# Kernel tuning notes

Hardware: AMD Instinct MI355X
Metric: run time of the kernel (lower is better)

The kernel has to match this reference:

```python
import jax, jax.numpy as jnp
import numpy as np

H = 96  # LSTM units hardcoded in the module


def setup_inputs() -> dict:
    key = jax.random.key(0)
    ks = jax.random.split(key, 5)
    B, LAT, V = 32, 64, 10000
    z = jax.random.normal(ks[0], (B, LAT), dtype=jnp.float32)
    # Keras LSTM params: kernel [in,4H], recurrent_kernel [H,4H], bias [4H]; gate order i,f,c,o
    W = jax.random.normal(ks[1], (LAT, 4 * H), dtype=jnp.float32) * 0.05
    U = jax.random.normal(ks[2], (H, 4 * H), dtype=jnp.float32) * 0.05
    b = jnp.zeros((4 * H,), dtype=jnp.float32)
    Wd = jax.random.normal(ks[3], (H, V), dtype=jnp.float32) * 0.05
    bd = jnp.zeros((V,), dtype=jnp.float32)
    return {"z": z, "W": W, "U": U, "b": b, "Wd": Wd, "bd": bd, "seq_len": 512}


def reference(z, W, U, b, Wd, bd, seq_len):
    # RepeatVector: every timestep sees the same input z, so the input
    # projection z@W + b is computed once and reused across all T steps.
    zp = z @ W + b  # [B, 4H]
    B = z.shape[0]
    h0 = jnp.zeros((B, H), z.dtype)
    c0 = jnp.zeros((B, H), z.dtype)

    def step(carry, _):
        h, c = carry
        g = zp + h @ U  # [B, 4H]
        i = jax.nn.sigmoid(g[:, :H])
        f = jax.nn.sigmoid(g[:, H:2 * H])
        cbar = jnp.tanh(g[:, 2 * H:3 * H])
        o = jax.nn.sigmoid(g[:, 3 * H:])
        c = f * c + i * cbar
        h = o * jnp.tanh(c)
        return (h, c), h

    _, hs = jax.lax.scan(step, (h0, c0), None, length=seq_len)  # [T, B, H]
    hs = jnp.transpose(hs, (1, 0, 2))  # [B, T, H]
    logits = hs @ Wd + bd  # [B, T, V]
    return jax.nn.softmax(logits, axis=-1)
```

## Files before the change

### kernel.cpp

```cpp
#include <hip/hip_runtime.h>
#include <cmath>

#define B_SZ  32
#define LATD  64
#define HU    96
#define G4    384
#define T_LEN 512
#define VOC   10000
#define NROWS (B_SZ * T_LEN)
#define NC16  625
#define NSPLIT 5
#define C16S  125
#define RBLK  32
#define PPR   (NSPLIT * 2)
#define HIST  256
#define PACK_BLOCKS ((NC16 * 3 * 64 + 383) / 384)
#define LSTM_GRID   (B_SZ + PACK_BLOCKS)

typedef __attribute__((ext_vector_type(8))) short bf16x8;
typedef __attribute__((ext_vector_type(4))) float f32x4;

__device__ __forceinline__ unsigned short f2bf(float x) {
  unsigned u = __float_as_uint(x);
  u += 0x7fffu + ((u >> 16) & 1u);
  return (unsigned short)(u >> 16);
}
__device__ __forceinline__ float fsig(float x) {
  return __builtin_amdgcn_rcpf(1.f + __expf(-x));
}
__device__ __forceinline__ float ftanh(float x) {
  return 1.f - 2.f * __builtin_amdgcn_rcpf(1.f + __expf(2.f * x));
}

__global__ __launch_bounds__(384) void lstm_fused(
    const float* __restrict__ z, const float* __restrict__ W,
    const float* __restrict__ U, const float* __restrict__ bias,
    const float* __restrict__ Wd, unsigned short* __restrict__ hsb,
    uint4* __restrict__ Bp) {
  const int tid = threadIdx.x;

  if (blockIdx.x >= B_SZ) {
    const int gid = (blockIdx.x - B_SZ) * 384 + tid;
    if (gid < NC16 * 3 * 64) {
      const int l   = gid & 63;
      const int K16 = (gid >> 6) % 3;
      const int c16 = gid / 192;
      const int col = c16 * 16 + (l & 15);
      const int k0  = K16 * 32 + (l >> 4) * 8;
      unsigned wb[4];
#pragma unroll
      for (int jj = 0; jj < 4; ++jj) {
        float x0 = Wd[(size_t)(k0 + 2 * jj) * VOC + col];
        float x1 = Wd[(size_t)(k0 + 2 * jj + 1) * VOC + col];
        wb[jj] = (unsigned)f2bf(x0) | ((unsigned)f2bf(x1) << 16);
      }
      Bp[gid] = make_uint4(wb[0], wb[1], wb[2], wb[3]);
    }
    return;
  }

  __shared__ __align__(16) unsigned short hsring[HIST][HU];
  __shared__ float z_lds[LATD];
  const int bb = blockIdx.x;
  const int l  = tid & 63, wv = tid >> 6;
  const int c  = l & 15, kg = l >> 4, k0 = kg * 8;

  if (tid < LATD) z_lds[tid] = z[bb * LATD + tid];
  if (tid < 12)   ((uint4*)(hsring[HIST - 1]))[tid] = make_uint4(0u, 0u, 0u, 0u);

  int cols[4];
#pragma unroll
  for (int g = 0; g < 4; ++g) cols[g] = (6 * g + wv) * 16 + c;

  bf16x8 Ufr[4][3];
#pragma unroll
  for (int g = 0; g < 4; ++g) {
#pragma unroll
    for (int kt = 0; kt < 3; ++kt) {
      const int kb = kt * 32 + k0;
      unsigned wb[4];
#pragma unroll
      for (int jj = 0; jj < 4; ++jj) {
        float x0 = U[(size_t)(kb + 2 * jj) * G4 + cols[g]];
        float x1 = U[(size_t)(kb + 2 * jj + 1) * G4 + cols[g]];
        wb[jj] = (unsigned)f2bf(x0) | ((unsigned)f2bf(x1) << 16);
      }
      uint4 u4 = make_uint4(wb[0], wb[1], wb[2], wb[3]);
      Ufr[g][kt] = __builtin_bit_cast(bf16x8, u4);
    }
  }

  float zp[4];
#pragma unroll
  for (int g = 0; g < 4; ++g) zp[g] = bias[cols[g]];
  __syncthreads();
  for (int k = 0; k < LATD; ++k) {
    const float zk = z_lds[k];
    const float* wr = W + (size_t)k * G4;
#pragma unroll
    for (int g = 0; g < 4; ++g) zp[g] = fmaf(zk, wr[cols[g]], zp[g]);
  }

  float cst = 0.f;
  unsigned short* hrow = hsb + (size_t)bb * T_LEN * HU;
  const f32x4 zero4 = {0.f, 0.f, 0.f, 0.f};
  const int u0 = c + 16 * wv;

  for (int s = 0; s < T_LEN; ++s) {
    const int rs = (s + HIST - 1) & (HIST - 1);
    bf16x8 afr[3];
#pragma unroll
    for (int kt = 0; kt < 3; ++kt)
      afr[kt] = *(const bf16x8*)(&hsring[rs][kt * 32 + k0]);

    float g4[4];
#pragma unroll
    for (int g = 0; g < 4; ++g) {
      f32x4 da = __builtin_amdgcn_mfma_f32_16x16x32_bf16(afr[0], Ufr[g][0], zero4, 0, 0, 0);
      da = __builtin_amdgcn_mfma_f32_16x16x32_bf16(afr[2], Ufr[g][2], da, 0, 0, 0);
      f32x4 db = __builtin_amdgcn_mfma_f32_16x16x32_bf16(afr[1], Ufr[g][1], zero4, 0, 0, 0);
      g4[g] = (da[0] + db[0]) + zp[g];
    }

    const float i_ = fsig(g4[0]);
    const float f_ = fsig(g4[1]);
    const float cb = ftanh(g4[2]);
    const float o_ = fsig(g4[3]);
    cst = f_ * cst + i_ * cb;
    const float h = o_ * ftanh(cst);
    if (kg == 0) hsring[s & (HIST - 1)][u0] = f2bf(h);
    __syncthreads();

    if ((s & (HIST - 1)) == (HIST - 1)) {
      const uint4* srcp = (const uint4*)hsring;
      uint4* dstp = (uint4*)(hrow + (size_t)(s - (HIST - 1)) * HU);
      for (int i = tid; i < HIST * HU / 8; i += 384) dstp[i] = srcp[i];
      __syncthreads();
    }
  }
}

template <int PASS>
__global__ __launch_bounds__(256) void dense_pass(
    const unsigned short* __restrict__ hsb, const bf16x8* __restrict__ Bp,
    const float* __restrict__ bd, const float* __restrict__ part,
    float* __restrict__ outp) {
  __shared__ __align__(16) unsigned short Al[RBLK * HU];
  const int tid = threadIdx.x;
  const int l = tid & 63, wv = tid >> 6;
  const int rt = wv & 1, cg = wv >> 1;
  const int l15 = l & 15, l4 = l >> 4;
  const int s = blockIdx.x / 512, rb = blockIdx.x % 512;
  const int R0 = rb * RBLK;

  {
    const uint4* src = (const uint4*)(hsb + (size_t)R0 * HU);
    uint4* dst = (uint4*)Al;
    for (int i = tid; i < RBLK * HU / 8; i += 256) dst[i] = src[i];
  }
  __syncthreads();

  bf16x8 afr[3];
#pragma unroll
  for (int kt = 0; kt < 3; ++kt)
    afr[kt] = *(const bf16x8*)(Al + (rt * 16 + l15) * HU + kt * 32 + l4 * 8);

  const int row = R0 + rt * 16 + l15;
  float iv = 0.f;
  if (PASS == 1) {
    float sum = 0.f;
#pragma unroll
    for (int i = 0; i < PPR; ++i) sum += part[(size_t)row * PPR + i];
    iv = 1.f / sum;
  }

  float srun = 0.f;
  for (int i = cg; i < C16S; i += 2) {
    const int c16 = s * C16S + i;
    const bf16x8* bp = Bp + (size_t)c16 * 192 + l;
    const bf16x8 b0 = bp[0], b1 = bp[64], b2 = bp[128];
    f32x4 acc = {0.f, 0.f, 0.f, 0.f};
    acc = __builtin_amdgcn_mfma_f32_16x16x32_bf16(b0, afr[0], acc, 0, 0, 0);
    acc = __builtin_amdgcn_mfma_f32_16x16x32_bf16(b1, afr[1], acc, 0, 0, 0);
    acc = __builtin_amdgcn_mfma_f32_16x16x32_bf16(b2, afr[2], acc, 0, 0, 0);
    const int colb = c16 * 16 + l4 * 4;
    const f32x4 bd4 = *(const f32x4*)(bd + colb);
    if (PASS == 0) {
#pragma unroll
      for (int q = 0; q < 4; ++q) srun += __expf(acc[q] + bd4[q]);
    } else {
      f32x4 o;
#pragma unroll
      for (int q = 0; q < 4; ++q) o[q] = __expf(acc[q] + bd4[q]) * iv;
      __builtin_nontemporal_store(o, (f32x4*)(outp + (size_t)row * VOC + colb));
    }
  }

  if (PASS == 0) {
    srun += __shfl_xor(srun, 16);
    srun += __shfl_xor(srun, 32);
    if (l4 == 0)
      ((float*)outp)[(size_t)row * PPR + s * 2 + cg] = srun;
  }
}

extern "C" void kernel_launch(void* const* d_in, const int* in_sizes, int n_in,
                              void* d_out, int out_size, void* d_ws, size_t ws_size,
                              hipStream_t stream) {
  const float* z  = (const float*)d_in[0];
  const float* W  = (const float*)d_in[1];
  const float* U  = (const float*)d_in[2];
  const float* b  = (const float*)d_in[3];
  const float* Wd = (const float*)d_in[4];
  const float* bd = (const float*)d_in[5];
  float* out = (float*)d_out;

  char* ws = (char*)d_ws;
  unsigned short* hsb = (unsigned short*)ws;
  uint4* Bp   = (uint4*)(ws + 3145728);
  float* part = (float*)(ws + 3145728 + 1920000);

  lstm_fused<<<LSTM_GRID, 384, 0, stream>>>(z, W, U, b, Wd, hsb, Bp);
  dense_pass<0><<<512 * NSPLIT, 256, 0, stream>>>(hsb, (const bf16x8*)Bp, bd,
                                                  nullptr, part);
  dense_pass<1><<<512 * NSPLIT, 256, 0, stream>>>(hsb, (const bf16x8*)Bp, bd,
                                                  part, out);
}
```

Measured before the change: 516.1 us.

## Split LSTM recurrence into halves and overlap dense passes with second half

The 512-step recurrence now runs as two 256-step kernels, carrying the cell state through a workspace buffer. The second LSTM half shares a launch with pass-0 softmax-sum blocks over the rows from the first half, and the remaining dense passes are spread across two more kernels. The gate scaling by log2e is folded into U and zp so the activations use exp2 directly, and the three MFMAs per gate no longer chain, which shortens the dependency on the serial path. The cost is more launches, extra state reloads, and dense blocks competing with the latency-bound LSTM blocks for CUs.

```diff
diff --git a/kernel.cpp b/kernel.cpp
--- a/kernel.cpp
+++ b/kernel.cpp
@@ -13,64 +13,48 @@
 #define C16S  125
 #define RBLK  32
 #define PPR   (NSPLIT * 2)
-#define HIST  256
-#define PACK_BLOCKS ((NC16 * 3 * 64 + 383) / 384)
-#define LSTM_GRID   (B_SZ + PACK_BLOCKS)
+#define HIST  64
+#define HALF  256
+#define PACK_BLOCKS 313
+#define D0H_BLOCKS  (256 * NSPLIT)
 
 typedef __attribute__((ext_vector_type(8))) short bf16x8;
 typedef __attribute__((ext_vector_type(4))) float f32x4;
+
+#define LOG2E  1.4426950408889634f
+#define LOG2E2 2.8853900817779268f
 
 __device__ __forceinline__ unsigned short f2bf(float x) {
   unsigned u = __float_as_uint(x);
   u += 0x7fffu + ((u >> 16) & 1u);
   return (unsigned short)(u >> 16);
 }
-__device__ __forceinline__ float fsig(float x) {
-  return __builtin_amdgcn_rcpf(1.f + __expf(-x));
-}
-__device__ __forceinline__ float ftanh(float x) {
-  return 1.f - 2.f * __builtin_amdgcn_rcpf(1.f + __expf(2.f * x));
-}
-
-__global__ __launch_bounds__(384) void lstm_fused(
+__device__ __forceinline__ float rcpf(float x) { return __builtin_amdgcn_rcpf(x); }
+__device__ __forceinline__ float exp2f_(float x) { return __builtin_amdgcn_exp2f(x); }
+
+__device__ __forceinline__ void lstm_body(
     const float* __restrict__ z, const float* __restrict__ W,
     const float* __restrict__ U, const float* __restrict__ bias,
-    const float* __restrict__ Wd, unsigned short* __restrict__ hsb,
-    uint4* __restrict__ Bp) {
+    unsigned short* __restrict__ hsb, float* __restrict__ c_save, int s0,
+    unsigned short (*ring)[HU], float* z_lds) {
   const int tid = threadIdx.x;
-
-  if (blockIdx.x >= B_SZ) {
-    const int gid = (blockIdx.x - B_SZ) * 384 + tid;
-    if (gid < NC16 * 3 * 64) {
-      const int l   = gid & 63;
-      const int K16 = (gid >> 6) % 3;
-      const int c16 = gid / 192;
-      const int col = c16 * 16 + (l & 15);
-      const int k0  = K16 * 32 + (l >> 4) * 8;
-      unsigned wb[4];
-#pragma unroll
-      for (int jj = 0; jj < 4; ++jj) {
-        float x0 = Wd[(size_t)(k0 + 2 * jj) * VOC + col];
-        float x1 = Wd[(size_t)(k0 + 2 * jj + 1) * VOC + col];
-        wb[jj] = (unsigned)f2bf(x0) | ((unsigned)f2bf(x1) << 16);
-      }
-      Bp[gid] = make_uint4(wb[0], wb[1], wb[2], wb[3]);
-    }
-    return;
-  }
-
-  __shared__ __align__(16) unsigned short hsring[HIST][HU];
-  __shared__ float z_lds[LATD];
-  const int bb = blockIdx.x;
-  const int l  = tid & 63, wv = tid >> 6;
-  const int c  = l & 15, kg = l >> 4, k0 = kg * 8;
+  const int bb  = blockIdx.x;
+  const int l   = tid & 63, wv = tid >> 6;
+  const int c   = l & 15, kg = l >> 4, k0 = kg * 8;
+  const int u0  = c + 16 * wv;
+  unsigned short* hrow = hsb + (size_t)bb * T_LEN * HU;
 
   if (tid < LATD) z_lds[tid] = z[bb * LATD + tid];
-  if (tid < 12)   ((uint4*)(hsring[HIST - 1]))[tid] = make_uint4(0u, 0u, 0u, 0u);
+  if (tid < 12) {
+    uint4 h0 = make_uint4(0u, 0u, 0u, 0u);
+    if (s0 != 0) h0 = ((const uint4*)(hrow + (size_t)(HALF - 1) * HU))[tid];
+    ((uint4*)(ring[HIST - 1]))[tid] = h0;
+  }
 
   int cols[4];
 #pragma unroll
   for (int g = 0; g < 4; ++g) cols[g] = (6 * g + wv) * 16 + c;
+  const float GS[4] = {-LOG2E, -LOG2E, LOG2E2, -LOG2E};
 
   bf16x8 Ufr[4][3];
 #pragma unroll
@@ -81,8 +65,8 @@
       unsigned wb[4];
 #pragma unroll
       for (int jj = 0; jj < 4; ++jj) {
-        float x0 = U[(size_t)(kb + 2 * jj) * G4 + cols[g]];
-        float x1 = U[(size_t)(kb + 2 * jj + 1) * G4 + cols[g]];
+        float x0 = U[(size_t)(kb + 2 * jj) * G4 + cols[g]] * GS[g];
+        float x1 = U[(size_t)(kb + 2 * jj + 1) * G4 + cols[g]] * GS[g];
         wb[jj] = (unsigned)f2bf(x0) | ((unsigned)f2bf(x1) << 16);
       }
       uint4 u4 = make_uint4(wb[0], wb[1], wb[2], wb[3]);
@@ -100,65 +84,64 @@
 #pragma unroll
     for (int g = 0; g < 4; ++g) zp[g] = fmaf(zk, wr[cols[g]], zp[g]);
   }
-
-  float cst = 0.f;
-  unsigned short* hrow = hsb + (size_t)bb * T_LEN * HU;
+#pragma unroll
+  for (int g = 0; g < 4; ++g) zp[g] *= GS[g];
+
+  float cst = (s0 == 0) ? 0.f : c_save[bb * HU + u0];
   const f32x4 zero4 = {0.f, 0.f, 0.f, 0.f};
-  const int u0 = c + 16 * wv;
-
-  for (int s = 0; s < T_LEN; ++s) {
-    const int rs = (s + HIST - 1) & (HIST - 1);
+
+  for (int ls = 0; ls < HALF; ++ls) {
+    const int rs = (ls + HIST - 1) & (HIST - 1);
     bf16x8 afr[3];
 #pragma unroll
     for (int kt = 0; kt < 3; ++kt)
-      afr[kt] = *(const bf16x8*)(&hsring[rs][kt * 32 + k0]);
-
-    float g4[4];
+      afr[kt] = *(const bf16x8*)(&ring[rs][kt * 32 + k0]);
+
+    float g4v[4];
 #pragma unroll
     for (int g = 0; g < 4; ++g) {
       f32x4 da = __builtin_amdgcn_mfma_f32_16x16x32_bf16(afr[0], Ufr[g][0], zero4, 0, 0, 0);
-      da = __builtin_amdgcn_mfma_f32_16x16x32_bf16(afr[2], Ufr[g][2], da, 0, 0, 0);
       f32x4 db = __builtin_amdgcn_mfma_f32_16x16x32_bf16(afr[1], Ufr[g][1], zero4, 0, 0, 0);
-      g4[g] = (da[0] + db[0]) + zp[g];
-    }
-
-    const float i_ = fsig(g4[0]);
-    const float f_ = fsig(g4[1]);
-    const float cb = ftanh(g4[2]);
-    const float o_ = fsig(g4[3]);
+      f32x4 dc = __builtin_amdgcn_mfma_f32_16x16x32_bf16(afr[2], Ufr[g][2], zero4, 0, 0, 0);
+      g4v[g] = (da[0] + db[0]) + (dc[0] + zp[g]);
+    }
+
+    const float i_ = rcpf(1.f + exp2f_(g4v[0]));
+    const float f_ = rcpf(1.f + exp2f_(g4v[1]));
+    const float cb = 1.f - 2.f * rcpf(1.f + exp2f_(g4v[2]));
+    const float o_ = rcpf(1.f + exp2f_(g4v[3]));
     cst = f_ * cst + i_ * cb;
-    const float h = o_ * ftanh(cst);
-    if (kg == 0) hsring[s & (HIST - 1)][u0] = f2bf(h);
+    const float th = 1.f - 2.f * rcpf(1.f + exp2f_(LOG2E2 * cst));
+    const float h  = o_ * th;
+    if (kg == 0) ring[ls & (HIST - 1)][u0] = f2bf(h);
     __syncthreads();
 
-    if ((s & (HIST - 1)) == (HIST - 1)) {
-      const uint4* srcp = (const uint4*)hsring;
-      uint4* dstp = (uint4*)(hrow + (size_t)(s - (HIST - 1)) * HU);
+    if ((ls & (HIST - 1)) == (HIST - 1)) {
+      const uint4* srcp = (const uint4*)ring;
+      uint4* dstp = (uint4*)(hrow + (size_t)(s0 + ls - (HIST - 1)) * HU);
       for (int i = tid; i < HIST * HU / 8; i += 384) dstp[i] = srcp[i];
       __syncthreads();
     }
   }
-}
-
-template <int PASS>
-__global__ __launch_bounds__(256) void dense_pass(
+  if (s0 == 0 && kg == 0) c_save[bb * HU + u0] = cst;
+}
+
+template <int PASS, int NT>
+__device__ __forceinline__ void dense_body(
     const unsigned short* __restrict__ hsb, const bf16x8* __restrict__ Bp,
     const float* __restrict__ bd, const float* __restrict__ part,
-    float* __restrict__ outp) {
-  __shared__ __align__(16) unsigned short Al[RBLK * HU];
-  const int tid = threadIdx.x;
+    float* __restrict__ outp, unsigned short* Al, int R0, int s, int tid) {
+  {
+    const uint4* src = (const uint4*)(hsb + (size_t)R0 * HU);
+    uint4* dst = (uint4*)Al;
+    for (int i = tid; i < RBLK * HU / 8; i += NT) dst[i] = src[i];
+  }
+  __syncthreads();
+  if (tid >= 256) return;
+
   const int l = tid & 63, wv = tid >> 6;
   const int rt = wv & 1, cg = wv >> 1;
   const int l15 = l & 15, l4 = l >> 4;
-  const int s = blockIdx.x / 512, rb = blockIdx.x % 512;
-  const int R0 = rb * RBLK;
-
-  {
-    const uint4* src = (const uint4*)(hsb + (size_t)R0 * HU);
-    uint4* dst = (uint4*)Al;
-    for (int i = tid; i < RBLK * HU / 8; i += 256) dst[i] = src[i];
-  }
-  __syncthreads();
 
   bf16x8 afr[3];
 #pragma unroll
@@ -204,6 +187,85 @@
   }
 }
 
+__device__ __forceinline__ int rb_of_half(int j, int hi) {
+  return (j >> 3) * 16 + hi * 8 + (j & 7);
+}
+
+__global__ __launch_bounds__(384) void k1_lstm_pack(
+    const float* __restrict__ z, const float* __restrict__ W,
+    const float* __restrict__ U, const float* __restrict__ bias,
+    const float* __restrict__ Wd, unsigned short* __restrict__ hsb,
+    uint4* __restrict__ Bp, float* __restrict__ c_save) {
+  if (blockIdx.x >= B_SZ) {
+    const int gid = (blockIdx.x - B_SZ) * 384 + threadIdx.x;
+    if (gid < NC16 * 3 * 64) {
+      const int l   = gid & 63;
+      const int K16 = (gid >> 6) % 3;
+      const int c16 = gid / 192;
+      const int col = c16 * 16 + (l & 15);
+      const int k0  = K16 * 32 + (l >> 4) * 8;
+      unsigned wb[4];
+#pragma unroll
+      for (int jj = 0; jj < 4; ++jj) {
+        float x0 = Wd[(size_t)(k0 + 2 * jj) * VOC + col];
+        float x1 = Wd[(size_t)(k0 + 2 * jj + 1) * VOC + col];
+        wb[jj] = (unsigned)f2bf(x0) | ((unsigned)f2bf(x1) << 16);
+      }
+      Bp[gid] = make_uint4(wb[0], wb[1], wb[2], wb[3]);
+    }
+    return;
+  }
+  __shared__ __align__(16) unsigned short ring[HIST][HU];
+  __shared__ float z_lds[LATD];
+  lstm_body(z, W, U, bias, hsb, c_save, 0, ring, z_lds);
+}
+
+__global__ __launch_bounds__(384) void k2_lstm_d0(
+    const float* __restrict__ z, const float* __restrict__ W,
+    const float* __restrict__ U, const float* __restrict__ bias,
+    unsigned short* __restrict__ hsb, const bf16x8* __restrict__ Bp,
+    const float* __restrict__ bd, float* __restrict__ part,
+    float* __restrict__ c_save) {
+  if (blockIdx.x >= B_SZ) {
+    __shared__ __align__(16) unsigned short Al[RBLK * HU];
+    const int db = blockIdx.x - B_SZ;
+    const int s = db / 256, j = db % 256;
+    dense_body<0, 384>(hsb, Bp, bd, nullptr, part, Al,
+                       rb_of_half(j, 0) * RBLK, s, threadIdx.x);
+    return;
+  }
+  __shared__ __align__(16) unsigned short ring[HIST][HU];
+  __shared__ float z_lds[LATD];
+  lstm_body(z, W, U, bias, hsb, c_save, HALF, ring, z_lds);
+}
+
+__global__ __launch_bounds__(256) void k3_d0_d1(
+    const unsigned short* __restrict__ hsb, const bf16x8* __restrict__ Bp,
+    const float* __restrict__ bd, float* __restrict__ part,
+    float* __restrict__ out) {
+  __shared__ __align__(16) unsigned short Al[RBLK * HU];
+  if (blockIdx.x < D0H_BLOCKS) {
+    const int s = blockIdx.x / 256, j = blockIdx.x % 256;
+    dense_body<0, 256>(hsb, Bp, bd, nullptr, part, Al,
+                       rb_of_half(j, 1) * RBLK, s, threadIdx.x);
+  } else {
+    const int db = blockIdx.x - D0H_BLOCKS;
+    const int s = db / 256, j = db % 256;
+    dense_body<1, 256>(hsb, Bp, bd, part, out, Al,
+                       rb_of_half(j, 0) * RBLK, s, threadIdx.x);
+  }
+}
+
+__global__ __launch_bounds__(256) void k4_d1(
+    const unsigned short* __restrict__ hsb, const bf16x8* __restrict__ Bp,
+    const float* __restrict__ bd, const float* __restrict__ part,
+    float* __restrict__ out) {
+  __shared__ __align__(16) unsigned short Al[RBLK * HU];
+  const int s = blockIdx.x / 256, j = blockIdx.x % 256;
+  dense_body<1, 256>(hsb, Bp, bd, part, out, Al,
+                     rb_of_half(j, 1) * RBLK, s, threadIdx.x);
+}
+
 extern "C" void kernel_launch(void* const* d_in, const int* in_sizes, int n_in,
                               void* d_out, int out_size, void* d_ws, size_t ws_size,
                               hipStream_t stream) {
@@ -217,12 +279,13 @@
 
   char* ws = (char*)d_ws;
   unsigned short* hsb = (unsigned short*)ws;
-  uint4* Bp   = (uint4*)(ws + 3145728);
-  float* part = (float*)(ws + 3145728 + 1920000);
-
-  lstm_fused<<<LSTM_GRID, 384, 0, stream>>>(z, W, U, b, Wd, hsb, Bp);
-  dense_pass<0><<<512 * NSPLIT, 256, 0, stream>>>(hsb, (const bf16x8*)Bp, bd,
-                                                  nullptr, part);
-  dense_pass<1><<<512 * NSPLIT, 256, 0, stream>>>(hsb, (const bf16x8*)Bp, bd,
-                                                  part, out);
-}
+  uint4* Bp    = (uint4*)(ws + 3145728);
+  float* part  = (float*)(ws + 3145728 + 1920000);
+  float* c_save = (float*)(ws + 3145728 + 1920000 + 655360);
+
+  k1_lstm_pack<<<B_SZ + PACK_BLOCKS, 384, 0, stream>>>(z, W, U, b, Wd, hsb, Bp, c_save);
+  k2_lstm_d0<<<B_SZ + D0H_BLOCKS, 384, 0, stream>>>(z, W, U, b, hsb,
+                                                    (const bf16x8*)Bp, bd, part, c_save);
+  k3_d0_d1<<<2 * D0H_BLOCKS, 256, 0, stream>>>(hsb, (const bf16x8*)Bp, bd, part, out);
+  k4_d1<<<D0H_BLOCKS, 256, 0, stream>>>(hsb, (const bf16x8*)Bp, bd, part, out);
+}
```

Measured after the change: 532.8 us. 1.03x slower.

## Batch 16 sequences per LSTM block using full MFMA rows

Applied to the files above, without the earlier changes.

The LSTM recurrence now runs 16 batch rows per block, filling the MFMA M dimension, so only 2 blocks run the serial recurrence where there were 32 blocks each using one row. Gate scaling by -log2e or 2log2e is folded into U and the input projection, so activations use exp2 directly. The history ring shrinks to 16 steps in a fragment-friendly layout that is flushed to global memory more often. The three MFMA chains are made independent to shorten dependency latency. The cost is more activation math per thread on each step.

```diff
diff --git a/kernel.cpp b/kernel.cpp
--- a/kernel.cpp
+++ b/kernel.cpp
@@ -1,5 +1,4 @@
 #include <hip/hip_runtime.h>
-#include <cmath>
 
 #define B_SZ  32
 #define LATD  64
@@ -13,35 +12,34 @@
 #define C16S  125
 #define RBLK  32
 #define PPR   (NSPLIT * 2)
-#define HIST  256
-#define PACK_BLOCKS ((NC16 * 3 * 64 + 383) / 384)
-#define LSTM_GRID   (B_SZ + PACK_BLOCKS)
+#define RING  16
+#define NPACK 313
+#define PACK_TOT (NC16 * 3 * 64)
 
 typedef __attribute__((ext_vector_type(8))) short bf16x8;
 typedef __attribute__((ext_vector_type(4))) float f32x4;
+
+#define LOG2E  1.4426950408889634f
+#define LOG2E2 2.8853900817779268f
 
 __device__ __forceinline__ unsigned short f2bf(float x) {
   unsigned u = __float_as_uint(x);
   u += 0x7fffu + ((u >> 16) & 1u);
   return (unsigned short)(u >> 16);
 }
-__device__ __forceinline__ float fsig(float x) {
-  return __builtin_amdgcn_rcpf(1.f + __expf(-x));
-}
-__device__ __forceinline__ float ftanh(float x) {
-  return 1.f - 2.f * __builtin_amdgcn_rcpf(1.f + __expf(2.f * x));
-}
-
-__global__ __launch_bounds__(384) void lstm_fused(
+__device__ __forceinline__ float rcpf_(float x) { return __builtin_amdgcn_rcpf(x); }
+__device__ __forceinline__ float exp2f_(float x) { return __builtin_amdgcn_exp2f(x); }
+
+__global__ __launch_bounds__(384) void k1_lstm_pack(
     const float* __restrict__ z, const float* __restrict__ W,
     const float* __restrict__ U, const float* __restrict__ bias,
     const float* __restrict__ Wd, unsigned short* __restrict__ hsb,
     uint4* __restrict__ Bp) {
   const int tid = threadIdx.x;
 
-  if (blockIdx.x >= B_SZ) {
-    const int gid = (blockIdx.x - B_SZ) * 384 + tid;
-    if (gid < NC16 * 3 * 64) {
+  if (blockIdx.x >= 2) {
+    const int gid = (blockIdx.x - 2) * 384 + tid;
+    if (gid < PACK_TOT) {
       const int l   = gid & 63;
       const int K16 = (gid >> 6) % 3;
       const int c16 = gid / 192;
@@ -59,30 +57,32 @@
     return;
   }
 
-  __shared__ __align__(16) unsigned short hsring[HIST][HU];
-  __shared__ float z_lds[LATD];
+  __shared__ __align__(16) unsigned short ring[RING][12][16][8];
+  __shared__ __align__(16) float z_lds[16][LATD];
   const int bb = blockIdx.x;
+  const int B0 = bb * 16;
   const int l  = tid & 63, wv = tid >> 6;
-  const int c  = l & 15, kg = l >> 4, k0 = kg * 8;
-
-  if (tid < LATD) z_lds[tid] = z[bb * LATD + tid];
-  if (tid < 12)   ((uint4*)(hsring[HIST - 1]))[tid] = make_uint4(0u, 0u, 0u, 0u);
+  const int c  = l & 15, kg = l >> 4;
+
+  if (tid < 256) ((uint4*)z_lds)[tid] = ((const uint4*)(z + B0 * LATD))[tid];
+  if (tid < 192) ((uint4*)ring[RING - 1])[tid] = make_uint4(0u, 0u, 0u, 0u);
 
   int cols[4];
 #pragma unroll
   for (int g = 0; g < 4; ++g) cols[g] = (6 * g + wv) * 16 + c;
+  const float GS[4] = {-LOG2E, -LOG2E, LOG2E2, -LOG2E};
 
   bf16x8 Ufr[4][3];
 #pragma unroll
   for (int g = 0; g < 4; ++g) {
 #pragma unroll
     for (int kt = 0; kt < 3; ++kt) {
-      const int kb = kt * 32 + k0;
+      const int kb = kt * 32 + kg * 8;
       unsigned wb[4];
 #pragma unroll
       for (int jj = 0; jj < 4; ++jj) {
-        float x0 = U[(size_t)(kb + 2 * jj) * G4 + cols[g]];
-        float x1 = U[(size_t)(kb + 2 * jj + 1) * G4 + cols[g]];
+        float x0 = U[(size_t)(kb + 2 * jj) * G4 + cols[g]] * GS[g];
+        float x1 = U[(size_t)(kb + 2 * jj + 1) * G4 + cols[g]] * GS[g];
         wb[jj] = (unsigned)f2bf(x0) | ((unsigned)f2bf(x1) << 16);
       }
       uint4 u4 = make_uint4(wb[0], wb[1], wb[2], wb[3]);
@@ -90,51 +90,74 @@
     }
   }
 
-  float zp[4];
-#pragma unroll
-  for (int g = 0; g < 4; ++g) zp[g] = bias[cols[g]];
   __syncthreads();
+
+  float zpv[4][4];
+#pragma unroll
+  for (int g = 0; g < 4; ++g) {
+    const float bv = bias[cols[g]];
+#pragma unroll
+    for (int q = 0; q < 4; ++q) zpv[g][q] = bv;
+  }
   for (int k = 0; k < LATD; ++k) {
-    const float zk = z_lds[k];
-    const float* wr = W + (size_t)k * G4;
-#pragma unroll
-    for (int g = 0; g < 4; ++g) zp[g] = fmaf(zk, wr[cols[g]], zp[g]);
-  }
-
-  float cst = 0.f;
-  unsigned short* hrow = hsb + (size_t)bb * T_LEN * HU;
+    float wk[4];
+#pragma unroll
+    for (int g = 0; g < 4; ++g) wk[g] = W[(size_t)k * G4 + cols[g]];
+#pragma unroll
+    for (int q = 0; q < 4; ++q) {
+      const float zq = z_lds[kg * 4 + q][k];
+#pragma unroll
+      for (int g = 0; g < 4; ++g) zpv[g][q] = fmaf(zq, wk[g], zpv[g][q]);
+    }
+  }
+#pragma unroll
+  for (int g = 0; g < 4; ++g)
+#pragma unroll
+    for (int q = 0; q < 4; ++q) zpv[g][q] *= GS[g];
+
+  f32x4 cst = {0.f, 0.f, 0.f, 0.f};
   const f32x4 zero4 = {0.f, 0.f, 0.f, 0.f};
-  const int u0 = c + 16 * wv;
-
-  for (int s = 0; s < T_LEN; ++s) {
-    const int rs = (s + HIST - 1) & (HIST - 1);
+  const int g8 = 2 * wv + (c >> 3), jj = c & 7;
+  uint4* dstb = (uint4*)hsb;
+
+  for (int ls = 0; ls < T_LEN; ++ls) {
+    const int rs = (ls + RING - 1) & (RING - 1);
     bf16x8 afr[3];
 #pragma unroll
     for (int kt = 0; kt < 3; ++kt)
-      afr[kt] = *(const bf16x8*)(&hsring[rs][kt * 32 + k0]);
-
-    float g4[4];
+      afr[kt] = *(const bf16x8*)(&ring[rs][kt * 4 + kg][c][0]);
+
+    f32x4 g4v[4];
 #pragma unroll
     for (int g = 0; g < 4; ++g) {
       f32x4 da = __builtin_amdgcn_mfma_f32_16x16x32_bf16(afr[0], Ufr[g][0], zero4, 0, 0, 0);
-      da = __builtin_amdgcn_mfma_f32_16x16x32_bf16(afr[2], Ufr[g][2], da, 0, 0, 0);
       f32x4 db = __builtin_amdgcn_mfma_f32_16x16x32_bf16(afr[1], Ufr[g][1], zero4, 0, 0, 0);
-      g4[g] = (da[0] + db[0]) + zp[g];
-    }
-
-    const float i_ = fsig(g4[0]);
-    const float f_ = fsig(g4[1]);
-    const float cb = ftanh(g4[2]);
-    const float o_ = fsig(g4[3]);
-    cst = f_ * cst + i_ * cb;
-    const float h = o_ * ftanh(cst);
-    if (kg == 0) hsring[s & (HIST - 1)][u0] = f2bf(h);
+      f32x4 dc = __builtin_amdgcn_mfma_f32_16x16x32_bf16(afr[2], Ufr[g][2], zero4, 0, 0, 0);
+#pragma unroll
+      for (int q = 0; q < 4; ++q)
+        g4v[g][q] = (da[q] + db[q]) + (dc[q] + zpv[g][q]);
+    }
+
+    const int ws_ = ls & (RING - 1);
+#pragma unroll
+    for (int q = 0; q < 4; ++q) {
+      const float i_ = rcpf_(1.f + exp2f_(g4v[0][q]));
+      const float f_ = rcpf_(1.f + exp2f_(g4v[1][q]));
+      const float cb = 1.f - 2.f * rcpf_(1.f + exp2f_(g4v[2][q]));
+      const float o_ = rcpf_(1.f + exp2f_(g4v[3][q]));
+      cst[q] = f_ * cst[q] + i_ * cb;
+      const float h = o_ * (1.f - 2.f * rcpf_(1.f + exp2f_(LOG2E2 * cst[q])));
+      ring[ws_][g8][kg * 4 + q][jj] = f2bf(h);
+    }
     __syncthreads();
 
-    if ((s & (HIST - 1)) == (HIST - 1)) {
-      const uint4* srcp = (const uint4*)hsring;
-      uint4* dstp = (uint4*)(hrow + (size_t)(s - (HIST - 1)) * HU);
-      for (int i = tid; i < HIST * HU / 8; i += 384) dstp[i] = srcp[i];
+    if ((ls & (RING - 1)) == (RING - 1)) {
+      const int s0 = ls - (RING - 1);
+      for (int i = tid; i < RING * 12 * 16; i += 384) {
+        const int slot = i / 192, g8i = (i / 16) % 12, ba = i & 15;
+        const uint4 v = *(const uint4*)(&ring[slot][g8i][ba][0]);
+        dstb[((size_t)(B0 + ba) * T_LEN + s0 + slot) * 12 + g8i] = v;
+      }
       __syncthreads();
     }
   }
@@ -220,7 +243,7 @@
   uint4* Bp   = (uint4*)(ws + 3145728);
   float* part = (float*)(ws + 3145728 + 1920000);
 
-  lstm_fused<<<LSTM_GRID, 384, 0, stream>>>(z, W, U, b, Wd, hsb, Bp);
+  k1_lstm_pack<<<2 + NPACK, 384, 0, stream>>>(z, W, U, b, Wd, hsb, Bp);
   dense_pass<0><<<512 * NSPLIT, 256, 0, stream>>>(hsb, (const bf16x8*)Bp, bd,
                                                   nullptr, part);
   dense_pass<1><<<512 * NSPLIT, 256, 0, stream>>>(hsb, (const bf16x8*)Bp, bd,
```

After: 844.9 us. 1.64x slower.
